# Performance work log

Hardware: AMD Instinct MI355X
Metric: run time of the kernel (lower is better)

Reference implementation:

```python
import jax, jax.numpy as jnp
import numpy as np

B, C, H, W = 4, 64, 128, 128
KH = KW = 3
K = KH * KW          # 9 neighbours
E = 64               # offset-cnn embedding channels
CK = C * K           # 576
MAX_DIST = 8.0
GROUPS = 1           # NonlocalBlock groups arg


def _conv(x, w, b=None, padding=0, groups=1):
    out = jax.lax.conv_general_dilated(
        x, w, (1, 1), [(padding, padding), (padding, padding)],
        dimension_numbers=('NCHW', 'OIHW', 'NCHW'), feature_group_count=groups)
    return out if b is None else out + b[None, :, None, None]


def _convnext(x, dw, pw1, pw2):
    y = _conv(x, dw, padding=3, groups=x.shape[1])
    y = _conv(jax.nn.relu(_conv(y, pw1)), pw2)
    return x + y


def _offset_cnn(x, ws, bs):
    y = jax.nn.leaky_relu(_conv(x, ws[0], bs[0]), 0.1)
    for i in range(1, 5):
        y = jax.nn.leaky_relu(_conv(y, ws[i], bs[i], padding=1), 0.1)
    return _conv(y, ws[5], bs[5])


def _deform_neighbourhood(x, offsets):
    # x: (B,C,H,W); offsets: (B, 2*K, H, W) as (k, [dy,dx]) pairs.
    b, c, h, w = x.shape
    off = offsets.reshape(b, K, 2, h, w)
    dy, dx = off[:, :, 0], off[:, :, 1]                       # (B,K,H,W)
    base = jnp.stack(jnp.meshgrid(jnp.arange(KH) - KH // 2,
                                  jnp.arange(KW) - KW // 2,
                                  indexing='ij'), 0).reshape(2, K).astype(x.dtype)
    hh = jnp.arange(h, dtype=x.dtype)[None, None, :, None]
    ww = jnp.arange(w, dtype=x.dtype)[None, None, None, :]
    py = hh + base[0][None, :, None, None] + dy               # (B,K,H,W)
    px = ww + base[1][None, :, None, None] + dx

    y0 = jnp.floor(py); x0 = jnp.floor(px)
    wy1 = py - y0; wy0 = 1.0 - wy1
    wx1 = px - x0; wx0 = 1.0 - wx1
    xf = x.reshape(b, c, h * w)

    def gather(yy, xx):
        valid = (yy >= 0) & (yy < h) & (xx >= 0) & (xx < w)
        yc = jnp.clip(yy, 0, h - 1).astype(jnp.int32)
        xc = jnp.clip(xx, 0, w - 1).astype(jnp.int32)
        idx = (yc * w + xc).reshape(b, -1)                    # (B, K*H*W)
        vals = jax.vmap(lambda m, i: m[:, i])(xf, idx)        # (B,C,K*H*W)
        return vals.reshape(b, c, K, h, w) * valid[:, None].astype(x.dtype)

    out = (gather(y0, x0) * (wy0 * wx0)[:, None]
           + gather(y0, x0 + 1) * (wy0 * wx1)[:, None]
           + gather(y0 + 1, x0) * (wy1 * wx0)[:, None]
           + gather(y0 + 1, x0 + 1) * (wy1 * wx1)[:, None])
    return out.reshape(b, c * K, h, w)                        # layout (feature, neighbour)


def _forward(x, enc_dw, enc_pw1, enc_pw2, dec_dw, dec_pw1, dec_pw2,
             off_w1, off_b1, off_w2, off_b2, off_w3, off_b3,
             off_w4, off_b4, off_w5, off_b5, off_w6, off_b6,
             dct_w, wie_w1, wie_w2, wie_w3, wie_w4, wie_w5, wie_w6,
             inv_w1, inv_w2):
    x = _convnext(x, enc_dw, enc_pw1, enc_pw2)
    offsets = MAX_DIST * jnp.tanh(_offset_cnn(
        x, [off_w1, off_w2, off_w3, off_w4, off_w5, off_w6],
        [off_b1, off_b2, off_b3, off_b4, off_b5, off_b6]))
    xb = _deform_neighbourhood(x, offsets)                    # (B, C*K, H, W)
    dct = _conv(xb, dct_w, groups=C // GROUPS)                # per-feature neighbour mixing
    y = _conv(xb, wie_w1)
    y = jax.nn.relu(_conv(y, wie_w2, padding=1, groups=CK))
    y = _conv(y, wie_w3)
    y = jax.nn.relu(_conv(y, wie_w4, padding=1, groups=CK))
    y = _conv(y, wie_w5)
    wiener = jax.nn.sigmoid(_conv(y, wie_w6, padding=1, groups=CK))
    out = _conv(_conv(wiener * dct, inv_w1, groups=C // GROUPS), inv_w2)
    return _convnext(out, dec_dw, dec_pw1, dec_pw2)


def setup_inputs() -> dict:
    key = jax.random.key(0)
    ks = iter(jax.random.split(key, 40))

    def w(shape, scale=None):
        fan_in = int(np.prod(shape[1:]))
        s = (1.0 / np.sqrt(fan_in)) if scale is None else scale
        return jax.random.normal(next(ks), shape, jnp.float32) * s

    inp = {
        'x': jax.random.normal(next(ks), (B, C, H, W), jnp.float32),
        'enc_dw': w((C, 1, 7, 7)), 'enc_pw1': w((2 * C, C, 1, 1)), 'enc_pw2': w((C, 2 * C, 1, 1)),
        'dec_dw': w((C, 1, 7, 7)), 'dec_pw1': w((2 * C, C, 1, 1)), 'dec_pw2': w((C, 2 * C, 1, 1)),
        'off_w1': w((E, C, 1, 1)), 'off_b1': w((E,), 0.01),
        'off_w2': w((E, E, 3, 3)), 'off_b2': w((E,), 0.01),
        'off_w3': w((E, E, 3, 3)), 'off_b3': w((E,), 0.01),
        'off_w4': w((E, E, 3, 3)), 'off_b4': w((E,), 0.01),
        'off_w5': w((E, E, 3, 3)), 'off_b5': w((E,), 0.01),
        'off_w6': w((2 * K, E, 1, 1), 0.02), 'off_b6': w((2 * K,), 0.01),
        'dct_w': w((CK, K, 1, 1)),
        'wie_w1': w((CK, CK, 1, 1)), 'wie_w2': w((CK, 1, 3, 3)),
        'wie_w3': w((CK, CK, 1, 1)), 'wie_w4': w((CK, 1, 3, 3)),
        'wie_w5': w((CK, CK, 1, 1)), 'wie_w6': w((CK, 1, 3, 3)),
        'inv_w1': w((CK, K, 1, 1)), 'inv_w2': w((C, CK, 1, 1)),
    }
    return inp


def reference(x, enc_dw, enc_pw1, enc_pw2, dec_dw, dec_pw1, dec_pw2,
              off_w1, off_b1, off_w2, off_b2, off_w3, off_b3,
              off_w4, off_b4, off_w5, off_b5, off_w6, off_b6,
              dct_w, wie_w1, wie_w2, wie_w3, wie_w4, wie_w5, wie_w6,
              inv_w1, inv_w2):
    return _forward(x, enc_dw, enc_pw1, enc_pw2, dec_dw, dec_pw1, dec_pw2,
                    off_w1, off_b1, off_w2, off_b2, off_w3, off_b3,
                    off_w4, off_b4, off_w5, off_b5, off_w6, off_b6,
                    dct_w, wie_w1, wie_w2, wie_w3, wie_w4, wie_w5, wie_w6,
                    inv_w1, inv_w2)
```

## Files before the change

kernel.cpp:

```cpp
#include <hip/hip_runtime.h>
#include <math.h>

#define HWp 16384
#define Wp 128
#define Hp 128
#define Bp 4
#define Cp 64
#define CKp 576

typedef unsigned int u32;
typedef unsigned short ushortt;
typedef __attribute__((ext_vector_type(8))) short short8;
typedef __attribute__((ext_vector_type(4))) float float4v;

__device__ __forceinline__ ushortt f2b(float f) {
  union { float f; u32 u; } x; x.f = f;
  u32 r = x.u + 0x7fff + ((x.u >> 16) & 1);
  return (ushortt)(r >> 16);
}
__device__ __forceinline__ float b2f(ushortt h) {
  union { u32 u; float f; } x; x.u = ((u32)h) << 16; return x.f;
}
__device__ __forceinline__ float blo(u32 t) {
  union { u32 u; float f; } x; x.u = t << 16; return x.f;
}
__device__ __forceinline__ float bhi(u32 t) {
  union { u32 u; float f; } x; x.u = t & 0xffff0000u; return x.f;
}
__device__ __forceinline__ void gll(const ushortt* g, ushortt* l) {
  __builtin_amdgcn_global_load_lds(
      (const __attribute__((address_space(1))) u32*)g,
      (__attribute__((address_space(3))) u32*)l, 16, 0, 0);
}

__global__ __launch_bounds__(256)
void dwconv7_lds(const float* __restrict__ in, const float* __restrict__ w,
                 float* __restrict__ out) {
  int bc = blockIdx.y;
  int tid = threadIdx.x;
  int y0 = blockIdx.x * 2;
  __shared__ float ws[49];
  __shared__ float tile[8][136];
  if (tid < 49) ws[tid] = w[(bc & 63) * 49 + tid];
  if (tid < 48) {
    int r = tid / 6, cc = tid % 6;
    tile[r][cc < 3 ? cc : 128 + cc] = 0.f;
  }
  const float* ip = in + (size_t)bc * HWp;
  #pragma unroll
  for (int i = 0; i < 4; i++) {
    int idx = tid + 256 * i;
    int r = idx >> 7, xx = idx & 127;
    int yy = y0 - 3 + r;
    tile[r][xx + 3] = (yy >= 0 && yy < Hp) ? ip[yy * Wp + xx] : 0.f;
  }
  __syncthreads();
  int ty = tid >> 7, x = tid & 127;
  float acc = 0.f;
  #pragma unroll
  for (int dy = 0; dy < 7; dy++)
    #pragma unroll
    for (int dx = 0; dx < 7; dx++)
      acc += tile[ty + dy][x + dx] * ws[dy * 7 + dx];
  out[(size_t)bc * HWp + (y0 + ty) * Wp + x] = acc;
}

template<int CIN, int ACT, int MODE>
__global__ __launch_bounds__(256)
void pw_bf(const ushortt* __restrict__ in, const ushortt* __restrict__ wt,
           const float* __restrict__ resid, void* __restrict__ outv, int Cout) {
  int tid = threadIdx.x;
  int wid = tid >> 6, lane = tid & 63;
  int q = lane >> 4, m = lane & 15;
  int px0 = blockIdx.x * 128, co0 = blockIdx.y * 64;
  int pxh = (wid & 1) * 64, coh = (wid >> 1) * 32;
  float4v acc[4][2];
  #pragma unroll
  for (int i = 0; i < 4; i++)
    #pragma unroll
    for (int j = 0; j < 2; j++) acc[i][j] = (float4v){0.f, 0.f, 0.f, 0.f};

  #pragma unroll
  for (int k0 = 0; k0 < CIN; k0 += 32) {
    short8 a[4], b[2];
    #pragma unroll
    for (int j = 0; j < 2; j++)
      b[j] = *(const short8*)&wt[(size_t)(co0 + coh + j * 16 + m) * CIN + k0 + q * 8];
    #pragma unroll
    for (int i = 0; i < 4; i++)
      a[i] = *(const short8*)&in[(size_t)(px0 + pxh + i * 16 + m) * CIN + k0 + q * 8];
    #pragma unroll
    for (int i = 0; i < 4; i++)
      #pragma unroll
      for (int j = 0; j < 2; j++)
        acc[i][j] = __builtin_amdgcn_mfma_f32_16x16x32_bf16(a[i], b[j], acc[i][j], 0, 0, 0);
  }

  #pragma unroll
  for (int j = 0; j < 2; j++) {
    int co = co0 + coh + j * 16 + m;
    #pragma unroll
    for (int i = 0; i < 4; i++) {
      int pxb = px0 + pxh + i * 16 + q * 4;
      int bl = pxb >> 14, pim = pxb & 16383;
      if (MODE == 0) {
        #pragma unroll
        for (int r = 0; r < 4; r++) {
          float v = acc[i][j][r];
          if (ACT == 1) v = fmaxf(v, 0.f);
          ((ushortt*)outv)[(size_t)(pxb + r) * Cout + co] = f2b(v);
        }
      } else {
        float4 rr = *(const float4*)&resid[(size_t)(bl * 64 + co) * HWp + pim];
        float v0 = acc[i][j][0] + rr.x, v1 = acc[i][j][1] + rr.y;
        float v2 = acc[i][j][2] + rr.z, v3 = acc[i][j][3] + rr.w;
        if (MODE == 1) {
          ushortt* ob = (ushortt*)outv;
          ob[(size_t)(pxb + 0) * 64 + co] = f2b(v0);
          ob[(size_t)(pxb + 1) * 64 + co] = f2b(v1);
          ob[(size_t)(pxb + 2) * 64 + co] = f2b(v2);
          ob[(size_t)(pxb + 3) * 64 + co] = f2b(v3);
        } else {
          float4 w4; w4.x = v0; w4.y = v1; w4.z = v2; w4.w = v3;
          *(float4*)&((float*)outv)[(size_t)(bl * 64 + co) * HWp + pim] = w4;
        }
      }
    }
  }
}

template<int TAPS>
__global__ __launch_bounds__(256)
void conv_bf(const ushortt* __restrict__ in, const ushortt* __restrict__ wt,
             const float* __restrict__ bias, ushortt* __restrict__ out) {
  int tid = threadIdx.x;
  int wid = tid >> 6, lane = tid & 63;
  int q = lane >> 4, m = lane & 15;
  int bx = blockIdx.x, b = blockIdx.y;
  int y = bx >> 1;
  int c0 = ((bx & 1) << 6) + ((wid & 1) << 5);
  int coW = (wid >> 1) << 5;
  size_t ibase = (size_t)b * HWp;

  float4v acc[2][2];
  #pragma unroll
  for (int i = 0; i < 2; i++)
    #pragma unroll
    for (int j = 0; j < 2; j++) acc[i][j] = (float4v){0.f, 0.f, 0.f, 0.f};
  short8 zz = {0, 0, 0, 0, 0, 0, 0, 0};

  #pragma unroll
  for (int k = 0; k < TAPS; k++) {
    int dy = (TAPS == 9) ? (k / 3 - 1) : 0;
    int dx = (TAPS == 9) ? (k % 3 - 1) : 0;
    int yy = y + dy;
    if (TAPS == 9 && (yy < 0 || yy >= Hp)) continue;
    #pragma unroll
    for (int ch = 0; ch < 2; ch++) {
      int ci0 = ch * 32 + q * 8;
      short8 bfr[2], afr[2];
      #pragma unroll
      for (int j = 0; j < 2; j++)
        bfr[j] = *(const short8*)&wt[(size_t)(k * 64 + coW + j * 16 + m) * 64 + ci0];
      #pragma unroll
      for (int i = 0; i < 2; i++) {
        int col = c0 + i * 16 + m + dx;
        bool vld = (TAPS == 1) || ((unsigned)col < (unsigned)Wp);
        int colc = min(max(col, 0), Wp - 1);
        short8 h = *(const short8*)&in[(ibase + (size_t)yy * Wp + colc) * 64 + ci0];
        afr[i] = vld ? h : zz;
      }
      #pragma unroll
      for (int i = 0; i < 2; i++)
        #pragma unroll
        for (int j = 0; j < 2; j++)
          acc[i][j] = __builtin_amdgcn_mfma_f32_16x16x32_bf16(afr[i], bfr[j], acc[i][j], 0, 0, 0);
    }
  }

  #pragma unroll
  for (int j = 0; j < 2; j++) {
    int co = coW + j * 16 + m;
    float bv = bias[co];
    #pragma unroll
    for (int i = 0; i < 2; i++) {
      #pragma unroll
      for (int r = 0; r < 4; r++) {
        size_t px = ibase + (size_t)y * Wp + c0 + i * 16 + q * 4 + r;
        float v = acc[i][j][r] + bv;
        v = v > 0.f ? v : 0.1f * v;
        out[px * 64 + co] = f2b(v);
      }
    }
  }
}

__global__ __launch_bounds__(256)
void t64b(const float* __restrict__ in, ushortt* __restrict__ out) {
  __shared__ float tl[64 * 65];
  int tid = threadIdx.x;
  int b = blockIdx.y;
  int px0 = blockIdx.x * 64;
  int lpx = tid & 63, c4 = tid >> 6;
  const float* ip = in + (size_t)b * 64 * HWp;
  #pragma unroll
  for (int i = 0; i < 16; i++) {
    int c = c4 + 4 * i;
    tl[lpx * 65 + c] = ip[(size_t)c * HWp + px0 + lpx];
  }
  __syncthreads();
  int ci = tid & 63, pr = tid >> 6;
  #pragma unroll
  for (int i = 0; i < 16; i++) {
    int r = pr + 4 * i;
    out[((size_t)b * HWp + px0 + r) * 64 + ci] = f2b(tl[r * 65 + ci]);
  }
}

__global__ __launch_bounds__(256)
void repw1(const float* __restrict__ in, ushortt* __restrict__ out) {
  int idx = blockIdx.x * 256 + threadIdx.x;
  if (idx >= 4096) return;
  out[idx] = f2b(in[idx]);
}
__global__ __launch_bounds__(256)
void repw9x4(const float* __restrict__ s0, const float* __restrict__ s1,
             const float* __restrict__ s2, const float* __restrict__ s3,
             ushortt* __restrict__ dst) {
  int which = blockIdx.y;
  const float* in = which == 0 ? s0 : which == 1 ? s1 : which == 2 ? s2 : s3;
  int idx = blockIdx.x * 256 + threadIdx.x;
  if (idx >= 36864) return;
  int k = idx >> 12, r = idx & 4095;
  int co = r >> 6, ci = r & 63;
  dst[which * 36864 + idx] = f2b(in[(size_t)(co * 64 + ci) * 9 + k]);
}
__global__ __launch_bounds__(256)
void rep576x3(const float* __restrict__ s0, const float* __restrict__ s1,
              const float* __restrict__ s2, ushortt* __restrict__ dst) {
  int which = blockIdx.y;
  const float* in = which == 0 ? s0 : which == 1 ? s1 : s2;
  int idx = blockIdx.x * 256 + threadIdx.x;
  if (idx >= 640 * 576) return;
  int cop = idx / 576, cip = idx % 576;
  ushortt v = 0;
  if (cop < 576) {
    int co = (cop & 63) * 9 + (cop >> 6);
    int ci = (cip & 63) * 9 + (cip >> 6);
    v = f2b(in[(size_t)co * 576 + ci]);
  }
  dst[(size_t)which * 640 * 576 + idx] = v;
}
__global__ __launch_bounds__(256)
void repinv2(const float* __restrict__ in, ushortt* __restrict__ out) {
  int idx = blockIdx.x * 256 + threadIdx.x;
  if (idx >= 64 * 576) return;
  int co = idx / 576, cip = idx % 576;
  int ci = (cip & 63) * 9 + (cip >> 6);
  out[idx] = f2b(in[(size_t)co * 576 + ci]);
}
__global__ __launch_bounds__(256)
void repdw3(const float* __restrict__ s0, const float* __restrict__ s1,
            const float* __restrict__ s2, ushortt* __restrict__ dst) {
  int idx = blockIdx.x * 256 + threadIdx.x;
  if (idx >= 3 * 5184) return;
  int which = idx / 5184, r = idx % 5184;
  const float* in = which == 0 ? s0 : which == 1 ? s1 : s2;
  int tap = r / 576, chp = r % 576;
  int ch = (chp & 63) * 9 + (chp >> 6);
  dst[idx] = f2b(in[ch * 9 + tap]);
}
__global__ __launch_bounds__(256)
void reppw4(const float* __restrict__ s0, const float* __restrict__ s1,
            const float* __restrict__ s2, const float* __restrict__ s3,
            ushortt* __restrict__ dst) {
  int which = blockIdx.y;
  const float* in = which == 0 ? s0 : which == 1 ? s1 : which == 2 ? s2 : s3;
  int idx = blockIdx.x * 256 + threadIdx.x;
  if (idx >= 8192) return;
  dst[which * 8192 + idx] = f2b(in[idx]);
}

__global__ __launch_bounds__(256)
void off6_nhwc(const ushortt* __restrict__ hi, const float* __restrict__ wgt,
               const float* __restrict__ bias, float* __restrict__ out) {
  __shared__ float Wl[18 * 64];
  for (int i = threadIdx.x; i < 18 * 64; i += 256) Wl[i] = wgt[i];
  __syncthreads();
  int px = blockIdx.x * 256 + threadIdx.x;
  int b = px >> 14, pim = px & 16383;
  float acc[18];
  #pragma unroll
  for (int j = 0; j < 18; j++) acc[j] = 0.f;
  const uint4* ph = (const uint4*)(hi + (size_t)px * 64);
  for (int g = 0; g < 8; g++) {
    uint4 H = ph[g];
    u32 hw[4] = {H.x, H.y, H.z, H.w};
    #pragma unroll
    for (int t = 0; t < 4; t++) {
      float v0 = blo(hw[t]);
      float v1 = bhi(hw[t]);
      int ci = g * 8 + t * 2;
      #pragma unroll
      for (int j = 0; j < 18; j++)
        acc[j] += Wl[j * 64 + ci] * v0 + Wl[j * 64 + ci + 1] * v1;
    }
  }
  #pragma unroll
  for (int j = 0; j < 18; j++)
    out[((size_t)b * 18 + j) * HWp + pim] = 8.f * tanhf(acc[j] + bias[j]);
}

__global__ __launch_bounds__(256)
void deform_dct(const ushortt* __restrict__ xn0, const float* __restrict__ offs0,
                const float* __restrict__ w9, ushortt* __restrict__ xb,
                ushortt* __restrict__ dctb) {
  __shared__ float Wl[5184];
  for (int i = threadIdx.x; i < 5184; i += 256) Wl[i] = w9[i];
  __syncthreads();
  int bl = blockIdx.y;
  const ushortt* xn = xn0 + (size_t)bl * HWp * 64;
  const float* offs = offs0 + (size_t)bl * 18 * HWp;
  int wid = threadIdx.x >> 6, lane = threadIdx.x & 63;
  int p = blockIdx.x * 4 + wid;
  int yi = p >> 7, xi = p & 127;
  size_t pg = (size_t)bl * HWp + p;
  float v[9];
  #pragma unroll
  for (int k = 0; k < 9; k++) {
    float dy = offs[(size_t)(2 * k) * HWp + p];
    float dx = offs[(size_t)(2 * k + 1) * HWp + p];
    float py = (float)yi + (float)(k / 3 - 1) + dy;
    float px = (float)xi + (float)(k % 3 - 1) + dx;
    float y0f = floorf(py), x0f = floorf(px);
    float wy1 = py - y0f, wy0 = 1.f - wy1;
    float wx1 = px - x0f, wx0 = 1.f - wx1;
    int y0 = (int)y0f, x0 = (int)x0f;
    bool vy0 = (y0 >= 0 && y0 < Hp), vy1 = (y0 + 1 >= 0 && y0 + 1 < Hp);
    bool vx0 = (x0 >= 0 && x0 < Wp), vx1 = (x0 + 1 >= 0 && x0 + 1 < Wp);
    int yc0 = min(max(y0, 0), Hp - 1), yc1 = min(max(y0 + 1, 0), Hp - 1);
    int xc0 = min(max(x0, 0), Wp - 1), xc1 = min(max(x0 + 1, 0), Wp - 1);
    float w00 = wy0 * wx0 * ((vy0 && vx0) ? 1.f : 0.f);
    float w01 = wy0 * wx1 * ((vy0 && vx1) ? 1.f : 0.f);
    float w10 = wy1 * wx0 * ((vy1 && vx0) ? 1.f : 0.f);
    float w11 = wy1 * wx1 * ((vy1 && vx1) ? 1.f : 0.f);
    float v00 = b2f(xn[(size_t)(yc0 * Wp + xc0) * 64 + lane]);
    float v01 = b2f(xn[(size_t)(yc0 * Wp + xc1) * 64 + lane]);
    float v10 = b2f(xn[(size_t)(yc1 * Wp + xc0) * 64 + lane]);
    float v11 = b2f(xn[(size_t)(yc1 * Wp + xc1) * 64 + lane]);
    v[k] = v00 * w00 + v01 * w01 + v10 * w10 + v11 * w11;
    xb[pg * 576 + 64 * k + lane] = f2b(v[k]);
  }
  const float* wc = &Wl[lane * 81];
  #pragma unroll
  for (int j = 0; j < 9; j++) {
    float a = 0.f;
    #pragma unroll
    for (int kk = 0; kk < 9; kk++) a += wc[j * 9 + kk] * v[kk];
    dctb[pg * 576 + 64 * j + lane] = f2b(a);
  }
}

__global__ __launch_bounds__(256)
void gemm128(const ushortt* __restrict__ X, const ushortt* __restrict__ Wb,
             ushortt* __restrict__ out) {
  __shared__ ushortt Xs[128 * 32];
  __shared__ ushortt Wsh[128 * 32];
  int tid = threadIdx.x;
  int lin = blockIdx.x + blockIdx.y * 5;
  int xcd = lin & 7, loc = lin >> 3;
  int co_t = loc % 5;
  int px_t = xcd * 32 + loc / 5;
  int co0 = co_t * 128, px0 = px_t * 128;
  int r0 = tid >> 2;
  int sch = (tid & 3) ^ ((tid >> 3) & 3);
  size_t gx0 = (size_t)(px0 + r0) * 576 + sch * 8;
  size_t gx1 = gx0 + (size_t)64 * 576;
  size_t gw0 = (size_t)(co0 + r0) * 576 + sch * 8;
  size_t gw1 = gw0 + (size_t)64 * 576;
  int wid = tid >> 6, lane = tid & 63;
  int q = lane >> 4, m = lane & 15;
  int qx = (q ^ ((m >> 1) & 3)) * 8;
  int pxh = (wid & 1) * 64, coh = (wid >> 1) * 64;
  float4v acc[4][4];
  #pragma unroll
  for (int i = 0; i < 4; i++)
    #pragma unroll
    for (int j = 0; j < 4; j++) acc[i][j] = (float4v){0.f, 0.f, 0.f, 0.f};

  for (int k0 = 0; k0 < 576; k0 += 32) {
    __syncthreads();
    gll(X + gx0 + k0,  &Xs[tid * 8]);
    gll(X + gx1 + k0,  &Xs[2048 + tid * 8]);
    gll(Wb + gw0 + k0, &Wsh[tid * 8]);
    gll(Wb + gw1 + k0, &Wsh[2048 + tid * 8]);
    __syncthreads();
    short8 a[4], b[4];
    #pragma unroll
    for (int i = 0; i < 4; i++)
      a[i] = *(const short8*)&Xs[(pxh + i * 16 + m) * 32 + qx];
    #pragma unroll
    for (int j = 0; j < 4; j++)
      b[j] = *(const short8*)&Wsh[(coh + j * 16 + m) * 32 + qx];
    #pragma unroll
    for (int i = 0; i < 4; i++)
      #pragma unroll
      for (int j = 0; j < 4; j++)
        acc[i][j] = __builtin_amdgcn_mfma_f32_16x16x32_bf16(a[i], b[j], acc[i][j], 0, 0, 0);
  }

  #pragma unroll
  for (int j = 0; j < 4; j++) {
    int co = co0 + coh + j * 16 + m;
    if (co >= 576) continue;
    #pragma unroll
    for (int i = 0; i < 4; i++) {
      int pxb = px0 + pxh + i * 16 + q * 4;
      #pragma unroll
      for (int r = 0; r < 4; r++)
        out[(size_t)(pxb + r) * 576 + co] = f2b(acc[i][j][r]);
    }
  }
}

__global__ __launch_bounds__(256)
void gemm64o2(const ushortt* __restrict__ X, const ushortt* __restrict__ Wb,
              float* __restrict__ outv) {
  __shared__ ushortt Xs[128 * 32];
  __shared__ ushortt Wsh[64 * 32];
  int tid = threadIdx.x;
  int px0 = (blockIdx.x + blockIdx.y * gridDim.x) * 128;
  int srow = tid >> 2;
  int sch = (tid & 3) ^ ((tid >> 3) & 3);
  size_t gxo0 = (size_t)(px0 + srow) * 576 + sch * 8;
  size_t gxo1 = gxo0 + (size_t)64 * 576;
  size_t gwo  = (size_t)srow * 576 + sch * 8;
  int wid = tid >> 6, lane = tid & 63;
  int q = lane >> 4, m = lane & 15;
  int qx = (q ^ ((m >> 1) & 3)) * 8;
  int pxh = (wid & 1) * 64, coh = (wid >> 1) * 32;
  float4v acc[4][2];
  #pragma unroll
  for (int i = 0; i < 4; i++)
    #pragma unroll
    for (int j = 0; j < 2; j++) acc[i][j] = (float4v){0.f, 0.f, 0.f, 0.f};

  for (int k0 = 0; k0 < 576; k0 += 32) {
    __syncthreads();
    gll(X + gxo0 + k0,  &Xs[tid * 8]);
    gll(X + gxo1 + k0,  &Xs[2048 + tid * 8]);
    gll(Wb + gwo + k0,  &Wsh[tid * 8]);
    __syncthreads();
    short8 a[4], b[2];
    #pragma unroll
    for (int i = 0; i < 4; i++)
      a[i] = *(const short8*)&Xs[(pxh + i * 16 + m) * 32 + qx];
    #pragma unroll
    for (int j = 0; j < 2; j++)
      b[j] = *(const short8*)&Wsh[(coh + j * 16 + m) * 32 + qx];
    #pragma unroll
    for (int i = 0; i < 4; i++)
      #pragma unroll
      for (int j = 0; j < 2; j++)
        acc[i][j] = __builtin_amdgcn_mfma_f32_16x16x32_bf16(a[i], b[j], acc[i][j], 0, 0, 0);
  }

  #pragma unroll
  for (int j = 0; j < 2; j++) {
    int co = coh + j * 16 + m;
    #pragma unroll
    for (int i = 0; i < 4; i++) {
      int pxb = px0 + pxh + i * 16 + q * 4;
      int bl = pxb >> 14, pim = pxb & 16383;
      float4 r;
      r.x = acc[i][j][0]; r.y = acc[i][j][1];
      r.z = acc[i][j][2]; r.w = acc[i][j][3];
      *(float4*)&outv[(size_t)(bl * 64 + co) * HWp + pim] = r;
    }
  }
}

template<int ACT>
__global__ __launch_bounds__(256)
void dw3x3_v2(const ushortt* __restrict__ in, const ushortt* __restrict__ wt,
              ushortt* __restrict__ out) {
  int tid = threadIdx.x;
  int pxl = tid / 72;
  int g = tid - pxl * 72;
  if (pxl >= 3) return;
  int x = blockIdx.x * 3 + pxl;
  if (x >= Wp) return;
  int y0 = blockIdx.y * 4;
  size_t bbase = (size_t)blockIdx.z * HWp;

  float w[9][8];
  #pragma unroll
  for (int t = 0; t < 9; t++) {
    uint4 wv = *(const uint4*)&wt[t * 576 + g * 8];
    u32 wsw[4] = {wv.x, wv.y, wv.z, wv.w};
    #pragma unroll
    for (int p = 0; p < 4; p++) {
      w[t][2 * p]     = blo(wsw[p]);
      w[t][2 * p + 1] = bhi(wsw[p]);
    }
  }
  float acc[4][8];
  #pragma unroll
  for (int o = 0; o < 4; o++)
    #pragma unroll
    for (int c = 0; c < 8; c++) acc[o][c] = 0.f;

  #pragma unroll
  for (int ri = 0; ri < 6; ri++) {
    int yy = y0 - 1 + ri;
    bool vr = (yy >= 0 && yy < Hp);
    float v[3][8];
    #pragma unroll
    for (int dx = 0; dx < 3; dx++) {
      int xx = x + dx - 1;
      uint4 t4 = {0, 0, 0, 0};
      if (vr && xx >= 0 && xx < Wp)
        t4 = *(const uint4*)&in[(bbase + (size_t)yy * Wp + xx) * 576 + g * 8];
      u32 tw[4] = {t4.x, t4.y, t4.z, t4.w};
      #pragma unroll
      for (int p = 0; p < 4; p++) {
        v[dx][2 * p]     = blo(tw[p]);
        v[dx][2 * p + 1] = bhi(tw[p]);
      }
    }
    #pragma unroll
    for (int o = 0; o < 4; o++) {
      int dy = ri - o;
      if (dy < 0 || dy > 2) continue;
      #pragma unroll
      for (int dx = 0; dx < 3; dx++)
        #pragma unroll
        for (int c = 0; c < 8; c++)
          acc[o][c] += w[dy * 3 + dx][c] * v[dx][c];
    }
  }

  #pragma unroll
  for (int o = 0; o < 4; o++) {
    int yy = y0 + o;
    u32 pk[4];
    #pragma unroll
    for (int p = 0; p < 4; p++) {
      float r0 = acc[o][2 * p], r1 = acc[o][2 * p + 1];
      if (ACT == 1) { r0 = fmaxf(r0, 0.f); r1 = fmaxf(r1, 0.f); }
      else { r0 = 1.f / (1.f + __expf(-r0)); r1 = 1.f / (1.f + __expf(-r1)); }
      pk[p] = (u32)f2b(r0) | (((u32)f2b(r1)) << 16);
    }
    uint4 o4; o4.x = pk[0]; o4.y = pk[1]; o4.z = pk[2]; o4.w = pk[3];
    *(uint4*)&out[(bbase + (size_t)yy * Wp + x) * 576 + g * 8] = o4;
  }
}

__global__ __launch_bounds__(256)
void g9inv(const ushortt* __restrict__ wien, const ushortt* __restrict__ dct,
           const float* __restrict__ w9, ushortt* __restrict__ outb) {
  __shared__ float Wl[5184];
  for (int i = threadIdx.x; i < 5184; i += 256) Wl[i] = w9[i];
  __syncthreads();
  int c = threadIdx.x & 63, pxl = threadIdx.x >> 6;
  size_t px = (size_t)blockIdx.x * 4 + pxl;
  float v[9];
  #pragma unroll
  for (int kk = 0; kk < 9; kk++)
    v[kk] = b2f(wien[px * 576 + 64 * kk + c]) * b2f(dct[px * 576 + 64 * kk + c]);
  const float* wc = &Wl[c * 81];
  #pragma unroll
  for (int j = 0; j < 9; j++) {
    float a = 0.f;
    #pragma unroll
    for (int kk = 0; kk < 9; kk++) a += wc[j * 9 + kk] * v[kk];
    outb[px * 576 + 64 * j + c] = f2b(a);
  }
}

extern "C" void kernel_launch(void* const* d_in, const int* in_sizes, int n_in,
                              void* d_out, int out_size, void* d_ws, size_t ws_size,
                              hipStream_t stream) {
  const float* x       = (const float*)d_in[0];
  const float* enc_dw  = (const float*)d_in[1];
  const float* enc_pw1 = (const float*)d_in[2];
  const float* enc_pw2 = (const float*)d_in[3];
  const float* dec_dw  = (const float*)d_in[4];
  const float* dec_pw1 = (const float*)d_in[5];
  const float* dec_pw2 = (const float*)d_in[6];
  const float* off_w1  = (const float*)d_in[7];
  const float* off_b1  = (const float*)d_in[8];
  const float* off_w2  = (const float*)d_in[9];
  const float* off_b2  = (const float*)d_in[10];
  const float* off_w3  = (const float*)d_in[11];
  const float* off_b3  = (const float*)d_in[12];
  const float* off_w4  = (const float*)d_in[13];
  const float* off_b4  = (const float*)d_in[14];
  const float* off_w5  = (const float*)d_in[15];
  const float* off_b5  = (const float*)d_in[16];
  const float* off_w6  = (const float*)d_in[17];
  const float* off_b6  = (const float*)d_in[18];
  const float* dct_w   = (const float*)d_in[19];
  const float* wie_w1  = (const float*)d_in[20];
  const float* wie_w2  = (const float*)d_in[21];
  const float* wie_w3  = (const float*)d_in[22];
  const float* wie_w4  = (const float*)d_in[23];
  const float* wie_w5  = (const float*)d_in[24];
  const float* wie_w6  = (const float*)d_in[25];
  const float* inv_w1  = (const float*)d_in[26];
  const float* inv_w2  = (const float*)d_in[27];
  float* outp = (float*)d_out;

  const size_t NP = (size_t)Bp * HWp;
  const size_t REQ_FLOATS = NP * 64 + NP * 64 + NP * 128 +
                            2 * (size_t)HWp * CKp + (size_t)HWp * CKp;
  if (ws_size < REQ_FLOATS * sizeof(float)) return;

  float* ws  = (float*)d_ws;
  float* x1  = ws;
  float* t0  = x1 + NP * 64;
  float* t1  = t0 + NP * 64;
  float* bigA = t1 + NP * 128;
  float* bigB = bigA + (size_t)HWp * CKp;
  float* bigC = bigB + (size_t)HWp * CKp;
  ushortt* R1 = (ushortt*)bigA;
  ushortt* R2 = (ushortt*)bigB;
  ushortt* R3 = (ushortt*)bigC;
  ushortt* e1 = (ushortt*)bigA;

  float* wreg = t0 + NP * 18;
  ushortt* wb  = (ushortt*)wreg;
  ushortt* wbi2 = wb + 3 * 640 * 576;
  ushortt* wdwb = wbi2 + 64 * 576;
  ushortt* wc1  = wdwb + 3 * 5184;
  ushortt* wc2  = wc1 + 4096;
  ushortt* wpw  = wc2 + 4 * 36864;

  ushortt* xnAll = (ushortt*)t1;
  ushortt* oA = xnAll + NP * 64;
  ushortt* oB = oA + NP * 64;

  float* offs = t0;
  float* mid  = x1;

  dim3 blk(256);

  dwconv7_lds<<<dim3(Hp / 2, Bp * Cp), blk, 0, stream>>>(x, enc_dw, t0);
  t64b<<<dim3(HWp / 64, Bp), blk, 0, stream>>>(t0, oA);

  rep576x3<<<dim3((640 * 576 + 255) / 256, 3), blk, 0, stream>>>(
      wie_w1, wie_w3, wie_w5, wb);
  repinv2<<<dim3((64 * 576 + 255) / 256), blk, 0, stream>>>(inv_w2, wbi2);
  repdw3<<<dim3((3 * 5184 + 255) / 256), blk, 0, stream>>>(wie_w2, wie_w4, wie_w6, wdwb);
  repw1<<<dim3(16), blk, 0, stream>>>(off_w1, wc1);
  repw9x4<<<dim3((36864 + 255) / 256, 4), blk, 0, stream>>>(
      off_w2, off_w3, off_w4, off_w5, wc2);
  reppw4<<<dim3(32, 4), blk, 0, stream>>>(enc_pw1, enc_pw2, dec_pw1, dec_pw2, wpw);

  pw_bf<64, 1, 0><<<dim3(NP / 128, 2), blk, 0, stream>>>(oA, wpw, nullptr, e1, 128);
  pw_bf<128, 0, 1><<<dim3(NP / 128, 1), blk, 0, stream>>>(e1, wpw + 8192, x, xnAll, 64);

  conv_bf<1><<<dim3(HWp / 64, Bp), blk, 0, stream>>>(xnAll, wc1, off_b1, oA);
  conv_bf<9><<<dim3(HWp / 64, Bp), blk, 0, stream>>>(oA, wc2,             off_b2, oB);
  conv_bf<9><<<dim3(HWp / 64, Bp), blk, 0, stream>>>(oB, wc2 + 36864,     off_b3, oA);
  conv_bf<9><<<dim3(HWp / 64, Bp), blk, 0, stream>>>(oA, wc2 + 2 * 36864, off_b4, oB);
  conv_bf<9><<<dim3(HWp / 64, Bp), blk, 0, stream>>>(oB, wc2 + 3 * 36864, off_b5, oA);
  off6_nhwc<<<dim3(NP / 256), blk, 0, stream>>>(oA, off_w6, off_b6, offs);

  for (int bp = 0; bp < 2; bp++) {
    const ushortt* xn0 = xnAll + (size_t)(2 * bp) * HWp * 64;
    const float* off0 = offs + (size_t)(2 * bp) * 18 * HWp;
    float* mid0 = mid + (size_t)(2 * bp) * 64 * HWp;

    deform_dct<<<dim3(HWp / 4, 2), blk, 0, stream>>>(xn0, off0, dct_w, R1, R2);
    gemm128<<<dim3(5, 256), blk, 0, stream>>>(R1, wb, R3);
    dw3x3_v2<1><<<dim3(43, 32, 2), blk, 0, stream>>>(R3, wdwb, R1);
    gemm128<<<dim3(5, 256), blk, 0, stream>>>(R1, wb + 640 * 576, R3);
    dw3x3_v2<1><<<dim3(43, 32, 2), blk, 0, stream>>>(R3, wdwb + 5184, R1);
    gemm128<<<dim3(5, 256), blk, 0, stream>>>(R1, wb + 2 * 640 * 576, R3);
    dw3x3_v2<2><<<dim3(43, 32, 2), blk, 0, stream>>>(R3, wdwb + 2 * 5184, R1);
    g9inv<<<dim3(2 * HWp / 4), blk, 0, stream>>>(R1, R2, inv_w1, R3);
    gemm64o2<<<dim3(1, 256), blk, 0, stream>>>(R3, wbi2, mid0);
  }

  dwconv7_lds<<<dim3(Hp / 2, Bp * Cp), blk, 0, stream>>>(mid, dec_dw, bigB);
  t64b<<<dim3(HWp / 64, Bp), blk, 0, stream>>>(bigB, oA);
  pw_bf<64, 1, 0><<<dim3(NP / 128, 2), blk, 0, stream>>>(oA, wpw + 2 * 8192, nullptr, e1, 128);
  pw_bf<128, 0, 2><<<dim3(NP / 128, 1), blk, 0, stream>>>(e1, wpw + 3 * 8192, mid, outp, 64);
}
```

Baseline: 928.2 us.

## Merge weight repacks, recompute DCT in inverse kernel, XCD-aware block remapping

Replaces six weight-repacking launches with one combined kernel to cut launch overhead. The deform kernel now only writes the sampled neighbourhood, using 2-channel packed loads and stores; the DCT of that neighbourhood is recomputed inside the inverse kernel instead of being stored and reloaded, which removes one 576-channel intermediate write and read. Several kernels also remap block indices so that neighbouring tiles land on the same XCD, aiming for better L2 locality. In exchange the inverse kernel does extra arithmetic and holds two weight tables in LDS, which may lower occupancy.

```diff
diff --git a/kernel.cpp b/kernel.cpp
--- a/kernel.cpp
+++ b/kernel.cpp
@@ -218,67 +218,69 @@
 }
 
 __global__ __launch_bounds__(256)
-void repw1(const float* __restrict__ in, ushortt* __restrict__ out) {
-  int idx = blockIdx.x * 256 + threadIdx.x;
-  if (idx >= 4096) return;
-  out[idx] = f2b(in[idx]);
-}
-__global__ __launch_bounds__(256)
-void repw9x4(const float* __restrict__ s0, const float* __restrict__ s1,
-             const float* __restrict__ s2, const float* __restrict__ s3,
-             ushortt* __restrict__ dst) {
-  int which = blockIdx.y;
-  const float* in = which == 0 ? s0 : which == 1 ? s1 : which == 2 ? s2 : s3;
-  int idx = blockIdx.x * 256 + threadIdx.x;
-  if (idx >= 36864) return;
-  int k = idx >> 12, r = idx & 4095;
-  int co = r >> 6, ci = r & 63;
-  dst[which * 36864 + idx] = f2b(in[(size_t)(co * 64 + ci) * 9 + k]);
-}
-__global__ __launch_bounds__(256)
-void rep576x3(const float* __restrict__ s0, const float* __restrict__ s1,
-              const float* __restrict__ s2, ushortt* __restrict__ dst) {
-  int which = blockIdx.y;
-  const float* in = which == 0 ? s0 : which == 1 ? s1 : s2;
-  int idx = blockIdx.x * 256 + threadIdx.x;
-  if (idx >= 640 * 576) return;
-  int cop = idx / 576, cip = idx % 576;
-  ushortt v = 0;
-  if (cop < 576) {
-    int co = (cop & 63) * 9 + (cop >> 6);
-    int ci = (cip & 63) * 9 + (cip >> 6);
-    v = f2b(in[(size_t)co * 576 + ci]);
-  }
-  dst[(size_t)which * 640 * 576 + idx] = v;
-}
-__global__ __launch_bounds__(256)
-void repinv2(const float* __restrict__ in, ushortt* __restrict__ out) {
-  int idx = blockIdx.x * 256 + threadIdx.x;
-  if (idx >= 64 * 576) return;
-  int co = idx / 576, cip = idx % 576;
-  int ci = (cip & 63) * 9 + (cip >> 6);
-  out[idx] = f2b(in[(size_t)co * 576 + ci]);
-}
-__global__ __launch_bounds__(256)
-void repdw3(const float* __restrict__ s0, const float* __restrict__ s1,
-            const float* __restrict__ s2, ushortt* __restrict__ dst) {
-  int idx = blockIdx.x * 256 + threadIdx.x;
-  if (idx >= 3 * 5184) return;
-  int which = idx / 5184, r = idx % 5184;
-  const float* in = which == 0 ? s0 : which == 1 ? s1 : s2;
-  int tap = r / 576, chp = r % 576;
-  int ch = (chp & 63) * 9 + (chp >> 6);
-  dst[idx] = f2b(in[ch * 9 + tap]);
-}
-__global__ __launch_bounds__(256)
-void reppw4(const float* __restrict__ s0, const float* __restrict__ s1,
-            const float* __restrict__ s2, const float* __restrict__ s3,
-            ushortt* __restrict__ dst) {
-  int which = blockIdx.y;
-  const float* in = which == 0 ? s0 : which == 1 ? s1 : which == 2 ? s2 : s3;
-  int idx = blockIdx.x * 256 + threadIdx.x;
-  if (idx >= 8192) return;
-  dst[which * 8192 + idx] = f2b(in[idx]);
+void repack_all(const float* __restrict__ w1a, const float* __restrict__ w3a,
+                const float* __restrict__ w5a, const float* __restrict__ inv2,
+                const float* __restrict__ d2, const float* __restrict__ d4,
+                const float* __restrict__ d6, const float* __restrict__ ow1,
+                const float* __restrict__ ow2, const float* __restrict__ ow3,
+                const float* __restrict__ ow4, const float* __restrict__ ow5,
+                const float* __restrict__ p1, const float* __restrict__ p2,
+                const float* __restrict__ p3, const float* __restrict__ p4,
+                ushortt* __restrict__ wb, ushortt* __restrict__ wbi2,
+                ushortt* __restrict__ wdwb, ushortt* __restrict__ wc1,
+                ushortt* __restrict__ wc2, ushortt* __restrict__ wpw) {
+  int b = blockIdx.x;
+  int tid = threadIdx.x;
+  if (b < 4320) {
+    int which = b / 1440;
+    int idx = (b - which * 1440) * 256 + tid;
+    const float* in = which == 0 ? w1a : which == 1 ? w3a : w5a;
+    int cop = idx / 576, cip = idx % 576;
+    ushortt v = 0;
+    if (cop < 576) {
+      int co = (cop & 63) * 9 + (cop >> 6);
+      int ci = (cip & 63) * 9 + (cip >> 6);
+      v = f2b(in[(size_t)co * 576 + ci]);
+    }
+    wb[(size_t)which * 640 * 576 + idx] = v;
+  } else if (b < 4464) {
+    int idx = (b - 4320) * 256 + tid;
+    if (idx < 64 * 576) {
+      int co = idx / 576, cip = idx % 576;
+      int ci = (cip & 63) * 9 + (cip >> 6);
+      wbi2[idx] = f2b(inv2[(size_t)co * 576 + ci]);
+    }
+  } else if (b < 4525) {
+    int idx = (b - 4464) * 256 + tid;
+    if (idx < 3 * 5184) {
+      int which = idx / 5184, r = idx % 5184;
+      const float* in = which == 0 ? d2 : which == 1 ? d4 : d6;
+      int tap = r / 576, chp = r % 576;
+      int ch = (chp & 63) * 9 + (chp >> 6);
+      wdwb[idx] = f2b(in[ch * 9 + tap]);
+    }
+  } else if (b < 4541) {
+    int idx = (b - 4525) * 256 + tid;
+    if (idx < 4096) wc1[idx] = f2b(ow1[idx]);
+  } else if (b < 5117) {
+    int bb = b - 4541;
+    int which = bb / 144;
+    int idx = (bb - which * 144) * 256 + tid;
+    if (idx < 36864) {
+      const float* in = which == 0 ? ow2 : which == 1 ? ow3 : which == 2 ? ow4 : ow5;
+      int k = idx >> 12, r = idx & 4095;
+      int co = r >> 6, ci = r & 63;
+      wc2[which * 36864 + idx] = f2b(in[(size_t)(co * 64 + ci) * 9 + k]);
+    }
+  } else {
+    int bb = b - 5117;
+    int which = bb / 32;
+    int idx = (bb - which * 32) * 256 + tid;
+    if (idx < 8192) {
+      const float* in = which == 0 ? p1 : which == 1 ? p2 : which == 2 ? p3 : p4;
+      wpw[which * 8192 + idx] = f2b(in[idx]);
+    }
+  }
 }
 
 __global__ __launch_bounds__(256)
@@ -312,20 +314,19 @@
 }
 
 __global__ __launch_bounds__(256)
-void deform_dct(const ushortt* __restrict__ xn0, const float* __restrict__ offs0,
-                const float* __restrict__ w9, ushortt* __restrict__ xb,
-                ushortt* __restrict__ dctb) {
-  __shared__ float Wl[5184];
-  for (int i = threadIdx.x; i < 5184; i += 256) Wl[i] = w9[i];
-  __syncthreads();
-  int bl = blockIdx.y;
+void deform_x(const ushortt* __restrict__ xn0, const float* __restrict__ offs0,
+              ushortt* __restrict__ xb) {
+  int lin = blockIdx.x;
+  int xcd = lin & 7, local = lin >> 3;
+  int rowi = local >> 4, bx = local & 15;
+  int tid = threadIdx.x;
+  int wid = tid >> 6, lane = tid & 63;
+  int c2 = lane & 31, ps = lane >> 5;
+  int pg = (xcd * 32 + rowi) * 128 + bx * 8 + wid * 2 + ps;
+  int bl = pg >> 14, p = pg & 16383;
   const ushortt* xn = xn0 + (size_t)bl * HWp * 64;
   const float* offs = offs0 + (size_t)bl * 18 * HWp;
-  int wid = threadIdx.x >> 6, lane = threadIdx.x & 63;
-  int p = blockIdx.x * 4 + wid;
   int yi = p >> 7, xi = p & 127;
-  size_t pg = (size_t)bl * HWp + p;
-  float v[9];
   #pragma unroll
   for (int k = 0; k < 9; k++) {
     float dy = offs[(size_t)(2 * k) * HWp + p];
@@ -344,20 +345,14 @@
     float w01 = wy0 * wx1 * ((vy0 && vx1) ? 1.f : 0.f);
     float w10 = wy1 * wx0 * ((vy1 && vx0) ? 1.f : 0.f);
     float w11 = wy1 * wx1 * ((vy1 && vx1) ? 1.f : 0.f);
-    float v00 = b2f(xn[(size_t)(yc0 * Wp + xc0) * 64 + lane]);
-    float v01 = b2f(xn[(size_t)(yc0 * Wp + xc1) * 64 + lane]);
-    float v10 = b2f(xn[(size_t)(yc1 * Wp + xc0) * 64 + lane]);
-    float v11 = b2f(xn[(size_t)(yc1 * Wp + xc1) * 64 + lane]);
-    v[k] = v00 * w00 + v01 * w01 + v10 * w10 + v11 * w11;
-    xb[pg * 576 + 64 * k + lane] = f2b(v[k]);
-  }
-  const float* wc = &Wl[lane * 81];
-  #pragma unroll
-  for (int j = 0; j < 9; j++) {
-    float a = 0.f;
-    #pragma unroll
-    for (int kk = 0; kk < 9; kk++) a += wc[j * 9 + kk] * v[kk];
-    dctb[pg * 576 + 64 * j + lane] = f2b(a);
+    u32 t00 = *(const u32*)&xn[(size_t)(yc0 * Wp + xc0) * 64 + c2 * 2];
+    u32 t01 = *(const u32*)&xn[(size_t)(yc0 * Wp + xc1) * 64 + c2 * 2];
+    u32 t10 = *(const u32*)&xn[(size_t)(yc1 * Wp + xc0) * 64 + c2 * 2];
+    u32 t11 = *(const u32*)&xn[(size_t)(yc1 * Wp + xc1) * 64 + c2 * 2];
+    float a = blo(t00) * w00 + blo(t01) * w01 + blo(t10) * w10 + blo(t11) * w11;
+    float bv = bhi(t00) * w00 + bhi(t01) * w01 + bhi(t10) * w10 + bhi(t11) * w11;
+    u32 pk = (u32)f2b(a) | (((u32)f2b(bv)) << 16);
+    *(u32*)&xb[(size_t)pg * 576 + 64 * k + c2 * 2] = pk;
   }
 }
 
@@ -429,7 +424,9 @@
   __shared__ ushortt Xs[128 * 32];
   __shared__ ushortt Wsh[64 * 32];
   int tid = threadIdx.x;
-  int px0 = (blockIdx.x + blockIdx.y * gridDim.x) * 128;
+  int lin = blockIdx.x;
+  int xcd = lin & 7, local = lin >> 3;
+  int px0 = (xcd * 32 + local) * 128;
   int srow = tid >> 2;
   int sch = (tid & 3) ^ ((tid >> 3) & 3);
   size_t gxo0 = (size_t)(px0 + srow) * 576 + sch * 8;
@@ -482,21 +479,26 @@
 
 template<int ACT>
 __global__ __launch_bounds__(256)
-void dw3x3_v2(const ushortt* __restrict__ in, const ushortt* __restrict__ wt,
+void dw3x3_v3(const ushortt* __restrict__ in, const ushortt* __restrict__ wt,
               ushortt* __restrict__ out) {
+  int lin = blockIdx.x;
+  int xcd = lin & 7, local = lin >> 3;
+  int g = local / 43, bxq = local - g * 43;
+  int rg = xcd * 8 + g;
+  int bz = rg >> 5, by = rg & 31;
   int tid = threadIdx.x;
   int pxl = tid / 72;
-  int g = tid - pxl * 72;
+  int gg = tid - pxl * 72;
   if (pxl >= 3) return;
-  int x = blockIdx.x * 3 + pxl;
+  int x = bxq * 3 + pxl;
   if (x >= Wp) return;
-  int y0 = blockIdx.y * 4;
-  size_t bbase = (size_t)blockIdx.z * HWp;
+  int y0 = by * 4;
+  size_t bbase = (size_t)bz * HWp;
 
   float w[9][8];
   #pragma unroll
   for (int t = 0; t < 9; t++) {
-    uint4 wv = *(const uint4*)&wt[t * 576 + g * 8];
+    uint4 wv = *(const uint4*)&wt[t * 576 + gg * 8];
     u32 wsw[4] = {wv.x, wv.y, wv.z, wv.w};
     #pragma unroll
     for (int p = 0; p < 4; p++) {
@@ -520,7 +522,7 @@
       int xx = x + dx - 1;
       uint4 t4 = {0, 0, 0, 0};
       if (vr && xx >= 0 && xx < Wp)
-        t4 = *(const uint4*)&in[(bbase + (size_t)yy * Wp + xx) * 576 + g * 8];
+        t4 = *(const uint4*)&in[(bbase + (size_t)yy * Wp + xx) * 576 + gg * 8];
       u32 tw[4] = {t4.x, t4.y, t4.z, t4.w};
       #pragma unroll
       for (int p = 0; p < 4; p++) {
@@ -552,28 +554,43 @@
       pk[p] = (u32)f2b(r0) | (((u32)f2b(r1)) << 16);
     }
     uint4 o4; o4.x = pk[0]; o4.y = pk[1]; o4.z = pk[2]; o4.w = pk[3];
-    *(uint4*)&out[(bbase + (size_t)yy * Wp + x) * 576 + g * 8] = o4;
-  }
-}
-
-__global__ __launch_bounds__(256)
-void g9inv(const ushortt* __restrict__ wien, const ushortt* __restrict__ dct,
-           const float* __restrict__ w9, ushortt* __restrict__ outb) {
-  __shared__ float Wl[5184];
-  for (int i = threadIdx.x; i < 5184; i += 256) Wl[i] = w9[i];
+    *(uint4*)&out[(bbase + (size_t)yy * Wp + x) * 576 + gg * 8] = o4;
+  }
+}
+
+__global__ __launch_bounds__(256)
+void g9inv2(const ushortt* __restrict__ wien, const ushortt* __restrict__ xb,
+            const float* __restrict__ wdct, const float* __restrict__ winv,
+            ushortt* __restrict__ outb) {
+  __shared__ float Wd[5184];
+  __shared__ float Wi[5184];
+  for (int i = threadIdx.x; i < 5184; i += 256) {
+    Wd[i] = wdct[i];
+    Wi[i] = winv[i];
+  }
   __syncthreads();
-  int c = threadIdx.x & 63, pxl = threadIdx.x >> 6;
-  size_t px = (size_t)blockIdx.x * 4 + pxl;
-  float v[9];
-  #pragma unroll
-  for (int kk = 0; kk < 9; kk++)
-    v[kk] = b2f(wien[px * 576 + 64 * kk + c]) * b2f(dct[px * 576 + 64 * kk + c]);
-  const float* wc = &Wl[c * 81];
+  int lin = blockIdx.x;
+  int xcd = lin & 7, local = lin >> 3;
+  int rowi = local >> 5, bx = local & 31;
+  size_t px = (size_t)((xcd * 32 + rowi) * 128 + bx * 4) + (threadIdx.x >> 6);
+  int c = threadIdx.x & 63;
+  float xr[9], v[9];
+  #pragma unroll
+  for (int t = 0; t < 9; t++) xr[t] = b2f(xb[px * 576 + 64 * t + c]);
+  const float* wd = &Wd[c * 81];
+  const float* wi = &Wi[c * 81];
+  #pragma unroll
+  for (int o = 0; o < 9; o++) {
+    float d = 0.f;
+    #pragma unroll
+    for (int t = 0; t < 9; t++) d += wd[o * 9 + t] * xr[t];
+    v[o] = b2f(wien[px * 576 + 64 * o + c]) * d;
+  }
   #pragma unroll
   for (int j = 0; j < 9; j++) {
     float a = 0.f;
     #pragma unroll
-    for (int kk = 0; kk < 9; kk++) a += wc[j * 9 + kk] * v[kk];
+    for (int o = 0; o < 9; o++) a += wi[j * 9 + o] * v[o];
     outb[px * 576 + 64 * j + c] = f2b(a);
   }
 }
@@ -648,14 +665,10 @@
   dwconv7_lds<<<dim3(Hp / 2, Bp * Cp), blk, 0, stream>>>(x, enc_dw, t0);
   t64b<<<dim3(HWp / 64, Bp), blk, 0, stream>>>(t0, oA);
 
-  rep576x3<<<dim3((640 * 576 + 255) / 256, 3), blk, 0, stream>>>(
-      wie_w1, wie_w3, wie_w5, wb);
-  repinv2<<<dim3((64 * 576 + 255) / 256), blk, 0, stream>>>(inv_w2, wbi2);
-  repdw3<<<dim3((3 * 5184 + 255) / 256), blk, 0, stream>>>(wie_w2, wie_w4, wie_w6, wdwb);
-  repw1<<<dim3(16), blk, 0, stream>>>(off_w1, wc1);
-  repw9x4<<<dim3((36864 + 255) / 256, 4), blk, 0, stream>>>(
-      off_w2, off_w3, off_w4, off_w5, wc2);
-  reppw4<<<dim3(32, 4), blk, 0, stream>>>(enc_pw1, enc_pw2, dec_pw1, dec_pw2, wpw);
+  repack_all<<<dim3(5245), blk, 0, stream>>>(
+      wie_w1, wie_w3, wie_w5, inv_w2, wie_w2, wie_w4, wie_w6, off_w1,
+      off_w2, off_w3, off_w4, off_w5, enc_pw1, enc_pw2, dec_pw1, dec_pw2,
+      wb, wbi2, wdwb, wc1, wc2, wpw);
 
   pw_bf<64, 1, 0><<<dim3(NP / 128, 2), blk, 0, stream>>>(oA, wpw, nullptr, e1, 128);
   pw_bf<128, 0, 1><<<dim3(NP / 128, 1), blk, 0, stream>>>(e1, wpw + 8192, x, xnAll, 64);
@@ -672,15 +685,15 @@
     const float* off0 = offs + (size_t)(2 * bp) * 18 * HWp;
     float* mid0 = mid + (size_t)(2 * bp) * 64 * HWp;
 
-    deform_dct<<<dim3(HWp / 4, 2), blk, 0, stream>>>(xn0, off0, dct_w, R1, R2);
-    gemm128<<<dim3(5, 256), blk, 0, stream>>>(R1, wb, R3);
-    dw3x3_v2<1><<<dim3(43, 32, 2), blk, 0, stream>>>(R3, wdwb, R1);
+    deform_x<<<dim3(4096), blk, 0, stream>>>(xn0, off0, R2);
+    gemm128<<<dim3(5, 256), blk, 0, stream>>>(R2, wb, R3);
+    dw3x3_v3<1><<<dim3(2752), blk, 0, stream>>>(R3, wdwb, R1);
     gemm128<<<dim3(5, 256), blk, 0, stream>>>(R1, wb + 640 * 576, R3);
-    dw3x3_v2<1><<<dim3(43, 32, 2), blk, 0, stream>>>(R3, wdwb + 5184, R1);
+    dw3x3_v3<1><<<dim3(2752), blk, 0, stream>>>(R3, wdwb + 5184, R1);
     gemm128<<<dim3(5, 256), blk, 0, stream>>>(R1, wb + 2 * 640 * 576, R3);
-    dw3x3_v2<2><<<dim3(43, 32, 2), blk, 0, stream>>>(R3, wdwb + 2 * 5184, R1);
-    g9inv<<<dim3(2 * HWp / 4), blk, 0, stream>>>(R1, R2, inv_w1, R3);
-    gemm64o2<<<dim3(1, 256), blk, 0, stream>>>(R3, wbi2, mid0);
+    dw3x3_v3<2><<<dim3(2752), blk, 0, stream>>>(R3, wdwb + 2 * 5184, R1);
+    g9inv2<<<dim3(8192), blk, 0, stream>>>(R1, R2, dct_w, inv_w1, R3);
+    gemm64o2<<<dim3(256), blk, 0, stream>>>(R3, wbi2, mid0);
   }
 
   dwconv7_lds<<<dim3(Hp / 2, Bp * Cp), blk, 0, stream>>>(mid, dec_dw, bigB);
```

Measured after the change: 898.9 us. 3.2% less time.
